# Performance work log

Hardware: AMD Instinct MI355X
Metric: run time of the kernel (lower is better)

## Reference

```python
import jax, jax.numpy as jnp
import numpy as np

OUT, IN, R = 8192, 8192, 16
GROUP = 16
SCALING = 16.0 / 16.0  # lora_alpha / r
# nvfp4 (e2m1) code table: 3 low bits magnitude, bit 3 = sign
NVFP4_LUT = jnp.array([0.0, 0.5, 1.0, 1.5, 2.0, 3.0, 4.0, 6.0,
                       -0.0, -0.5, -1.0, -1.5, -2.0, -3.0, -4.0, -6.0],
                      dtype=jnp.float32)


def setup_inputs() -> dict:
    key = jax.random.key(0)
    k1, k2, k3, k4, k5 = jax.random.split(key, 5)
    x = jax.random.normal(k1, (64, IN), dtype=jnp.float32)
    packed_weight = jax.random.randint(k2, (OUT, IN // 2), 0, 256, dtype=jnp.int32).astype(jnp.uint8)
    # effective block scales (global scale already absorbed, as in _load_prequantized_nvfp4)
    weight_block_scales = (jax.random.uniform(k3, (OUT, IN // GROUP), dtype=jnp.float32) + 0.1) * 0.01
    lora_A = jax.random.normal(k4, (R, IN), dtype=jnp.float32) * (1.0 / np.sqrt(IN))
    lora_B = jax.random.normal(k5, (OUT, R), dtype=jnp.float32) * 0.01
    return {"x": x, "packed_weight": packed_weight,
            "weight_block_scales": weight_block_scales,
            "lora_A": lora_A, "lora_B": lora_B}


def _dequant_nvfp4(packed, block_scales):
    # packed: (OUT, IN//2) uint8, two fp4 codes per byte (low nibble = even index)
    low = (packed & 0xF).astype(jnp.int32)
    high = (packed >> 4).astype(jnp.int32)
    codes = jnp.stack([low, high], axis=-1).reshape(packed.shape[0], -1)  # (OUT, IN)
    vals = NVFP4_LUT[codes]
    O, I = vals.shape
    # per-block scale over groups of GROUP along in_features
    W = (vals.reshape(O, I // GROUP, GROUP) * block_scales[:, :, None]).reshape(O, I)
    return W


def reference(x, packed_weight, weight_block_scales, lora_A, lora_B):
    W = _dequant_nvfp4(packed_weight, weight_block_scales)      # (OUT, IN) fp32
    base = x @ W.T                                              # (B, OUT)
    lora = (x @ lora_A.T) @ lora_B.T                            # (B, OUT)
    return base + SCALING * lora
```

## Files before the change

kernel.cpp:

```cpp
#include <hip/hip_runtime.h>
#include <stdint.h>

#define IN_F   8192
#define OUT_F  8192
#define MB     64
#define RANK   16
#define KSPLIT 16
#define KSTEPS 16

typedef _Float16 f16x8 __attribute__((ext_vector_type(8)));
typedef _Float16 f16x2 __attribute__((ext_vector_type(2)));
typedef float    f32x4 __attribute__((ext_vector_type(4)));

__device__ __forceinline__ unsigned pk2h(float a, float b) {
    return __builtin_bit_cast(unsigned, __builtin_amdgcn_cvt_pkrtz(a, b));
}

__device__ __forceinline__ f16x8 decode8(unsigned p, unsigned s2) {
    unsigned q  = p >> 4;
    unsigned me = __builtin_amdgcn_perm(0x46444240u, 0x3E3C3800u, p & 0x07070707u);
    unsigned mo = __builtin_amdgcn_perm(0x46444240u, 0x3E3C3800u, q & 0x07070707u);
    unsigned he = ((p & 0x08080808u) << 4) | me;
    unsigned ho = ((q & 0x08080808u) << 4) | mo;
    unsigned bu0 = __builtin_amdgcn_perm(ho, he, 0x040C000Cu);
    unsigned bu1 = __builtin_amdgcn_perm(ho, he, 0x050C010Cu);
    unsigned bu2 = __builtin_amdgcn_perm(ho, he, 0x060C020Cu);
    unsigned bu3 = __builtin_amdgcn_perm(ho, he, 0x070C030Cu);
    f16x2 sv = __builtin_bit_cast(f16x2, s2);
    f16x2 h0 = __builtin_bit_cast(f16x2, bu0) * sv;
    f16x2 h1 = __builtin_bit_cast(f16x2, bu1) * sv;
    f16x2 h2 = __builtin_bit_cast(f16x2, bu2) * sv;
    f16x2 h3 = __builtin_bit_cast(f16x2, bu3) * sv;
    f16x8 b;
    b[0]=h0[0]; b[1]=h0[1]; b[2]=h1[0]; b[3]=h1[1];
    b[4]=h2[0]; b[5]=h2[1]; b[6]=h3[0]; b[7]=h3[1];
    return b;
}

__global__ void detect_kernel(const unsigned* __restrict__ Wp,
                              int* __restrict__ flag, float* __restrict__ t) {
    unsigned v = Wp[threadIdx.x & 63];
    unsigned long long m = __ballot(v > 255u);
    if (threadIdx.x == 0) *flag = (m == 0ull) ? 1 : 0;
    for (int i = threadIdx.x; i < MB * RANK; i += 256) t[i] = 0.f;
}

__global__ __launch_bounds__(256) void prep_kernel(
    const float* __restrict__ x, const float* __restrict__ lora_A,
    uint2* __restrict__ xf2, float* __restrict__ t)
{
    const int m = blockIdx.x, kq = blockIdx.y;
    const int tid = threadIdx.x;
    const int mt = m >> 4, l15 = m & 15;
    float acc[RANK];
#pragma unroll
    for (int r = 0; r < RANK; ++r) acc[r] = 0.f;

    const float4* x4 = (const float4*)(x + (size_t)m * IN_F);
    const float4* A4 = (const float4*)lora_A;
#pragma unroll
    for (int it = 0; it < 2; ++it) {
        int j = kq * 512 + it * 256 + tid;
        float4 xv = x4[j];
        uint2 u;
        u.x = pk2h(xv.x, xv.y);
        u.y = pk2h(xv.z, xv.w);
        int kstep = j >> 3, quad = (j >> 1) & 3, h = j & 1;
        xf2[(size_t)(((kstep * 4 + mt) * 64 + quad * 16 + l15) * 2 + h)] = u;
#pragma unroll
        for (int r = 0; r < RANK; ++r) {
            float4 av = A4[(size_t)r * (IN_F / 4) + j];
            acc[r] += xv.x * av.x + xv.y * av.y + xv.z * av.z + xv.w * av.w;
        }
    }
#pragma unroll
    for (int r = 0; r < RANK; ++r)
#pragma unroll
        for (int off = 32; off > 0; off >>= 1)
            acc[r] += __shfl_down(acc[r], off);

    __shared__ float red[4][RANK];
    int lane = tid & 63, wid = tid >> 6;
    if (lane == 0) {
#pragma unroll
        for (int r = 0; r < RANK; ++r) red[wid][r] = acc[r];
    }
    __syncthreads();
    if (tid < RANK)
        atomicAdd(&t[m * RANK + tid],
                  red[0][tid] + red[1][tid] + red[2][tid] + red[3][tid]);
}

__device__ __forceinline__ float4 lora4(const float* __restrict__ t, int m,
                                        const float* __restrict__ lora_B, int n4) {
    const float4* t4 = (const float4*)(t + m * RANK);
    float4 ta = t4[0], tb = t4[1], tc = t4[2], td = t4[3];
    float4 o;
    float* op = (float*)&o;
#pragma unroll
    for (int j = 0; j < 4; ++j) {
        const float4* B4 = (const float4*)(lora_B + (size_t)(n4 + j) * RANK);
        float4 b0 = B4[0], b1 = B4[1], b2 = B4[2], b3 = B4[3];
        op[j] = ta.x * b0.x + ta.y * b0.y + ta.z * b0.z + ta.w * b0.w
              + tb.x * b1.x + tb.y * b1.y + tb.z * b1.z + tb.w * b1.w
              + tc.x * b2.x + tc.y * b2.y + tc.z * b2.z + tc.w * b2.w
              + td.x * b3.x + td.y * b3.y + td.z * b3.z + td.w * b3.w;
    }
    return o;
}

__global__ __launch_bounds__(256) void lora_kernel(
    const float* __restrict__ t, const float* __restrict__ lora_B,
    float* __restrict__ out)
{
    const int gid = blockIdx.x * 256 + threadIdx.x;
    ((float4*)out)[gid] = lora4(t, gid >> 11, lora_B, (gid & 2047) * 4);
}

__global__ __launch_bounds__(256) void finish_kernel(
    const float* __restrict__ partial, const float* __restrict__ t,
    const float* __restrict__ lora_B, float* __restrict__ out)
{
    const int gid = blockIdx.x * 256 + threadIdx.x;
    float4 p = {0.f, 0.f, 0.f, 0.f};
#pragma unroll
    for (int ksp = 0; ksp < KSPLIT; ++ksp) {
        float4 v = ((const float4*)partial)[(size_t)ksp * (MB * OUT_F / 4) + gid];
        p.x += v.x; p.y += v.y; p.z += v.z; p.w += v.w;
    }
    float4 l = lora4(t, gid >> 11, lora_B, (gid & 2047) * 4);
    p.x += l.x; p.y += l.y; p.z += l.z; p.w += l.w;
    ((float4*)out)[gid] = p;
}

template<int FMT, int ATOMIC>
__global__ __launch_bounds__(512, 4) void main_kernel(
    const void*  __restrict__ Wpv,
    const float* __restrict__ scales,
    const uint4* __restrict__ xf4,
    const int*   __restrict__ flag,
    float*       __restrict__ dst)
{
    if (*flag != FMT) return;

    __shared__ __align__(16) char xs[65536];

    const int tid = threadIdx.x;
    const int lane = tid & 63, w = tid >> 6;
    const int l15 = lane & 15, quad = lane >> 4, qh = quad >> 1;
    const int ks = blockIdx.x;
    const int n0 = blockIdx.y * 256 + w * 32;
    const int row = n0 + l15;

    {
        const uint4* gsrc = xf4 + (size_t)ks * (KSTEPS * 4 * 64);
#pragma unroll
        for (int i = 0; i < 8; ++i) {
            int idx = i * 512 + tid;
            uint4 v = gsrc[idx];
            *(uint4*)&xs[(size_t)idx * 16] = v;
        }
    }
    __syncthreads();

    f32x4 acc[4][2];
#pragma unroll
    for (int mt = 0; mt < 4; ++mt)
#pragma unroll
        for (int nt = 0; nt < 2; ++nt)
            acc[mt][nt] = (f32x4){0.f, 0.f, 0.f, 0.f};

    const uint4*    wi0 = (const uint4*)Wpv + (size_t)row * (IN_F / 8) + ks * 64 + quad;
    const uint4*    wi1 = wi0 + (size_t)16 * (IN_F / 8);
    const unsigned* wb0 = (const unsigned*)Wpv + (size_t)row * (IN_F / 8) + ks * 64 + quad;
    const unsigned* wb1 = wb0 + (size_t)16 * (IN_F / 8);
    const float4*   sp4 = (const float4*)(scales + (size_t)row * (IN_F / 16) + ks * 32);
    const float4*   sq4 = (const float4*)(scales + (size_t)(row + 16) * (IN_F / 16) + ks * 32);

    uint4    wv[2][2][4];
    unsigned wp[2][2][4];
    float4   sc[2][2][2];

#define LOADCH(buf, c)                                                   \
    do {                                                                 \
        _Pragma("unroll")                                                \
        for (int j = 0; j < 4; ++j) {                                    \
            if (FMT == 1) {                                              \
                wv[buf][0][j] = wi0[((c) * 4 + j) * 4];                  \
                wv[buf][1][j] = wi1[((c) * 4 + j) * 4];                  \
            } else {                                                     \
                wp[buf][0][j] = wb0[((c) * 4 + j) * 4];                  \
                wp[buf][1][j] = wb1[((c) * 4 + j) * 4];                  \
            }                                                            \
        }                                                                \
        sc[buf][0][0] = sp4[(c) * 2]; sc[buf][0][1] = sp4[(c) * 2 + 1];  \
        sc[buf][1][0] = sq4[(c) * 2]; sc[buf][1][1] = sq4[(c) * 2 + 1];  \
    } while (0)

    LOADCH(0, 0);
    LOADCH(1, 1);

#pragma unroll
    for (int c = 0; c < 4; ++c) {
        const int buf = c & 1;
#pragma unroll
        for (int j = 0; j < 4; ++j) {
            const int s = c * 4 + j;
            f16x8 afr[4];
#pragma unroll
            for (int mt = 0; mt < 4; ++mt)
                afr[mt] = *(const f16x8*)&xs[(size_t)(((s * 4 + mt) * 64) + lane) * 16];
#pragma unroll
            for (int nt = 0; nt < 2; ++nt) {
                float4 v = sc[buf][nt][j >> 1];
                float scf = (j & 1) ? (qh ? v.w : v.z) : (qh ? v.y : v.x);
                unsigned s2 = pk2h(scf, scf);
                unsigned p;
                if (FMT == 1) {
                    uint4 u = wv[buf][nt][j];
                    p = u.x | (u.y << 8) | (u.z << 16) | (u.w << 24);
                } else {
                    p = wp[buf][nt][j];
                }
                f16x8 b = decode8(p, s2);
#pragma unroll
                for (int mt = 0; mt < 4; ++mt)
                    acc[mt][nt] = __builtin_amdgcn_mfma_f32_16x16x32_f16(
                        afr[mt], b, acc[mt][nt], 0, 0, 0);
            }
        }
        if (c < 2) LOADCH(buf, c + 2);
    }
#undef LOADCH

    if (ATOMIC == 0) {
        float* pb = dst + (size_t)ks * (MB * OUT_F);
#pragma unroll
        for (int mt = 0; mt < 4; ++mt)
#pragma unroll
            for (int nt = 0; nt < 2; ++nt)
#pragma unroll
                for (int r = 0; r < 4; ++r)
                    pb[(size_t)(mt * 16 + quad * 4 + r) * OUT_F + n0 + nt * 16 + l15]
                        = acc[mt][nt][r];
    } else {
#pragma unroll
        for (int mt = 0; mt < 4; ++mt)
#pragma unroll
            for (int nt = 0; nt < 2; ++nt)
#pragma unroll
                for (int r = 0; r < 4; ++r)
                    atomicAdd(&dst[(size_t)(mt * 16 + quad * 4 + r) * OUT_F
                                   + n0 + nt * 16 + l15], acc[mt][nt][r]);
    }
}

extern "C" void kernel_launch(void* const* d_in, const int* in_sizes, int n_in,
                              void* d_out, int out_size, void* d_ws, size_t ws_size,
                              hipStream_t stream)
{
    (void)in_sizes; (void)n_in; (void)out_size;
    const float* x      = (const float*)d_in[0];
    const void*  Wp     = (const void*)d_in[1];
    const float* scales = (const float*)d_in[2];
    const float* lora_A = (const float*)d_in[3];
    const float* lora_B = (const float*)d_in[4];
    float* out = (float*)d_out;

    char* ws = (char*)d_ws;
    int*   flag    = (int*)ws;
    float* t       = (float*)(ws + 4096);
    uint2* xf      = (uint2*)(ws + 65536);
    float* partial = (float*)(ws + (2u << 20));

    const bool big_ws = ws_size >= ((size_t)34 << 20);

    detect_kernel<<<1, 256, 0, stream>>>((const unsigned*)Wp, flag, t);
    prep_kernel<<<dim3(64, 4), 256, 0, stream>>>(x, lora_A, xf, t);

    if (big_ws) {
        main_kernel<1, 0><<<dim3(KSPLIT, 32), 512, 0, stream>>>(
            Wp, scales, (const uint4*)xf, flag, partial);
        main_kernel<0, 0><<<dim3(KSPLIT, 32), 512, 0, stream>>>(
            Wp, scales, (const uint4*)xf, flag, partial);
        finish_kernel<<<(MB * OUT_F / 4) / 256, 256, 0, stream>>>(
            partial, t, lora_B, out);
    } else {
        lora_kernel<<<(MB * OUT_F / 4) / 256, 256, 0, stream>>>(t, lora_B, out);
        main_kernel<1, 1><<<dim3(KSPLIT, 32), 512, 0, stream>>>(
            Wp, scales, (const uint4*)xf, flag, out);
        main_kernel<0, 1><<<dim3(KSPLIT, 32), 512, 0, stream>>>(
            Wp, scales, (const uint4*)xf, flag, out);
    }
}
```

Measured before the change: 246.6 us.

## Stream packed weights via global_load_lds into per-wave LDS ring buffers

Weight fetches now go through async global-to-LDS loads (global_load_lds) into a per-wave double-buffered LDS region. An explicit vmcnt wait gates each of eight smaller chunks, instead of holding weight chunks in registers. Block scales are loaded once up front and pre-packed to half2 registers. The aim is to cut VGPR pressure and keep more loads in flight. In exchange it adds 64KB more LDS per block, which can reduce occupancy under the 512-thread, 4-blocks launch bound, and it relies on hand-coded waitcnt values being correct.

```diff
diff --git a/kernel.cpp b/kernel.cpp
--- a/kernel.cpp
+++ b/kernel.cpp
@@ -15,6 +15,18 @@
 __device__ __forceinline__ unsigned pk2h(float a, float b) {
     return __builtin_bit_cast(unsigned, __builtin_amdgcn_cvt_pkrtz(a, b));
 }
+
+__device__ __forceinline__ void glds16(const void* gp, void* lp) {
+    __builtin_amdgcn_global_load_lds(
+        (const __attribute__((address_space(1))) void*)gp,
+        (__attribute__((address_space(3))) void*)lp, 16, 0, 0);
+}
+__device__ __forceinline__ void glds4(const void* gp, void* lp) {
+    __builtin_amdgcn_global_load_lds(
+        (const __attribute__((address_space(1))) void*)gp,
+        (__attribute__((address_space(3))) void*)lp, 4, 0, 0);
+}
+#define MEMBAR() __asm__ __volatile__("" ::: "memory")
 
 __device__ __forceinline__ f16x8 decode8(unsigned p, unsigned s2) {
     unsigned q  = p >> 4;
@@ -144,6 +156,7 @@
     if (*flag != FMT) return;
 
     __shared__ __align__(16) char xs[65536];
+    __shared__ __align__(16) char wl[65536];
 
     const int tid = threadIdx.x;
     const int lane = tid & 63, w = tid >> 6;
@@ -152,6 +165,23 @@
     const int n0 = blockIdx.y * 256 + w * 32;
     const int row = n0 + l15;
 
+    unsigned sreg[2][KSTEPS];
+    {
+        const float4* sp0 = (const float4*)(scales + (size_t)row * (IN_F / 16) + ks * 32);
+        const float4* sp1 = (const float4*)(scales + (size_t)(row + 16) * (IN_F / 16) + ks * 32);
+#pragma unroll
+        for (int nt = 0; nt < 2; ++nt) {
+            const float4* sp = nt ? sp1 : sp0;
+#pragma unroll
+            for (int i = 0; i < 8; ++i) {
+                float4 v = sp[i];
+                float a = qh ? v.y : v.x, b = qh ? v.w : v.z;
+                sreg[nt][2 * i]     = pk2h(a, a);
+                sreg[nt][2 * i + 1] = pk2h(b, b);
+            }
+        }
+    }
+
     {
         const uint4* gsrc = xf4 + (size_t)ks * (KSTEPS * 4 * 64);
 #pragma unroll
@@ -170,68 +200,57 @@
         for (int nt = 0; nt < 2; ++nt)
             acc[mt][nt] = (f32x4){0.f, 0.f, 0.f, 0.f};
 
-    const uint4*    wi0 = (const uint4*)Wpv + (size_t)row * (IN_F / 8) + ks * 64 + quad;
-    const uint4*    wi1 = wi0 + (size_t)16 * (IN_F / 8);
-    const unsigned* wb0 = (const unsigned*)Wpv + (size_t)row * (IN_F / 8) + ks * 64 + quad;
-    const unsigned* wb1 = wb0 + (size_t)16 * (IN_F / 8);
-    const float4*   sp4 = (const float4*)(scales + (size_t)row * (IN_F / 16) + ks * 32);
-    const float4*   sq4 = (const float4*)(scales + (size_t)(row + 16) * (IN_F / 16) + ks * 32);
-
-    uint4    wv[2][2][4];
-    unsigned wp[2][2][4];
-    float4   sc[2][2][2];
-
-#define LOADCH(buf, c)                                                   \
-    do {                                                                 \
-        _Pragma("unroll")                                                \
-        for (int j = 0; j < 4; ++j) {                                    \
-            if (FMT == 1) {                                              \
-                wv[buf][0][j] = wi0[((c) * 4 + j) * 4];                  \
-                wv[buf][1][j] = wi1[((c) * 4 + j) * 4];                  \
-            } else {                                                     \
-                wp[buf][0][j] = wb0[((c) * 4 + j) * 4];                  \
-                wp[buf][1][j] = wb1[((c) * 4 + j) * 4];                  \
-            }                                                            \
-        }                                                                \
-        sc[buf][0][0] = sp4[(c) * 2]; sc[buf][0][1] = sp4[(c) * 2 + 1];  \
-        sc[buf][1][0] = sq4[(c) * 2]; sc[buf][1][1] = sq4[(c) * 2 + 1];  \
+    char* wlw = &wl[(size_t)w * 8192];
+
+#define ISSUE(c, buf)                                                        \
+    do {                                                                     \
+        _Pragma("unroll") for (int j = 0; j < 2; ++j)                        \
+        _Pragma("unroll") for (int nt = 0; nt < 2; ++nt) {                   \
+            size_t e = (size_t)(row + nt * 16) * 1024                        \
+                       + (ks * 64 + ((c) * 2 + j) * 4 + quad);               \
+            char* ldst = &wlw[(size_t)((buf) * 4 + j * 2 + nt) * 1024];      \
+            if (FMT == 1) glds16((const char*)Wpv + e * 16, ldst);           \
+            else          glds4 ((const char*)Wpv + e * 4,  ldst);           \
+        }                                                                    \
     } while (0)
 
-    LOADCH(0, 0);
-    LOADCH(1, 1);
-
-#pragma unroll
-    for (int c = 0; c < 4; ++c) {
+    ISSUE(0, 0);
+    ISSUE(1, 1);
+
+#pragma unroll
+    for (int c = 0; c < 8; ++c) {
         const int buf = c & 1;
-#pragma unroll
-        for (int j = 0; j < 4; ++j) {
-            const int s = c * 4 + j;
+        MEMBAR();
+        if (c < 7) __builtin_amdgcn_s_waitcnt(0x0F74);
+        else       __builtin_amdgcn_s_waitcnt(0x0F70);
+        MEMBAR();
+#pragma unroll
+        for (int j = 0; j < 2; ++j) {
+            const int s = c * 2 + j;
             f16x8 afr[4];
 #pragma unroll
             for (int mt = 0; mt < 4; ++mt)
-                afr[mt] = *(const f16x8*)&xs[(size_t)(((s * 4 + mt) * 64) + lane) * 16];
+                afr[mt] = *(const f16x8*)&xs[(size_t)((s * 4 + mt) * 64 + lane) * 16];
 #pragma unroll
             for (int nt = 0; nt < 2; ++nt) {
-                float4 v = sc[buf][nt][j >> 1];
-                float scf = (j & 1) ? (qh ? v.w : v.z) : (qh ? v.y : v.x);
-                unsigned s2 = pk2h(scf, scf);
+                const char* slot = &wlw[(size_t)(buf * 4 + j * 2 + nt) * 1024];
                 unsigned p;
                 if (FMT == 1) {
-                    uint4 u = wv[buf][nt][j];
+                    uint4 u = *(const uint4*)(slot + (size_t)lane * 16);
                     p = u.x | (u.y << 8) | (u.z << 16) | (u.w << 24);
                 } else {
-                    p = wp[buf][nt][j];
+                    p = *(const unsigned*)(slot + (size_t)lane * 4);
                 }
-                f16x8 b = decode8(p, s2);
+                f16x8 b = decode8(p, sreg[nt][s]);
 #pragma unroll
                 for (int mt = 0; mt < 4; ++mt)
                     acc[mt][nt] = __builtin_amdgcn_mfma_f32_16x16x32_f16(
                         afr[mt], b, acc[mt][nt], 0, 0, 0);
             }
         }
-        if (c < 2) LOADCH(buf, c + 2);
-    }
-#undef LOADCH
+        if (c < 6) { MEMBAR(); ISSUE(c + 2, buf); }
+    }
+#undef ISSUE
 
     if (ATOMIC == 0) {
         float* pb = dst + (size_t)ks * (MB * OUT_F);
```

New measurement: 241.2 us. -2.2%, faster.
